# Kernel optimization log

Hardware: AMD Instinct MI355X
Metric: run time of the kernel (lower is better)

## Reference

```python
import jax, jax.numpy as jnp
from jax import lax
import numpy as np

D_MODEL = 1024
D_STATE = 16
D_CONV = 4
EXPAND = 2
D_INNER = EXPAND * D_MODEL  # 2048
DT_RANK = D_MODEL // 16     # 64
BATCH = 4
SEQ = 1024


def setup_inputs() -> dict:
    key = jax.random.key(0)
    ks = iter(jax.random.split(key, 40))
    def w(shape, s=0.02):
        return (s * jax.random.normal(next(ks), shape)).astype(jnp.float32)
    inp = {"x": jax.random.normal(next(ks), (BATCH, SEQ, D_MODEL), dtype=jnp.float32)}
    # S4D-real style A init: A = -exp(A_log), A_log = log(1..N) per channel
    Alog = jnp.log(jnp.tile(jnp.arange(1, D_STATE + 1, dtype=jnp.float32), (D_INNER, 1)))
    for s in ("f", "b"):
        inp[f"inproj_{s}"] = w((D_MODEL, 2 * D_INNER))
        inp[f"conv_w_{s}"] = w((D_INNER, D_CONV), 0.2)
        inp[f"conv_b_{s}"] = jnp.zeros((D_INNER,), jnp.float32)
        inp[f"xproj_{s}"] = w((D_INNER, DT_RANK + 2 * D_STATE))
        inp[f"dt_w_{s}"] = w((DT_RANK, D_INNER))
        inp[f"dt_b_{s}"] = jnp.full((D_INNER,), -4.0, jnp.float32)  # softplus(-4)~0.018
        inp[f"Alog_{s}"] = Alog
        inp[f"Dp_{s}"] = jnp.ones((D_INNER,), jnp.float32)
        inp[f"outproj_{s}"] = w((D_INNER, D_MODEL))
    inp["gate_w"] = w((2 * D_MODEL, D_MODEL))
    inp["gate_b"] = jnp.zeros((D_MODEL,), jnp.float32)
    inp["proj_w"] = w((D_MODEL, D_MODEL))
    inp["proj_b"] = jnp.zeros((D_MODEL,), jnp.float32)
    return inp


def _mamba(x, inproj, conv_w, conv_b, xproj, dt_w, dt_b, Alog, Dp, outproj):
    B, L, _ = x.shape
    xz = x @ inproj                           # [B,L,2*Di]
    u, z = jnp.split(xz, 2, axis=-1)          # each [B,L,Di]
    # depthwise causal conv1d, width D_CONV
    K = conv_w.shape[1]
    up = jnp.pad(u, ((0, 0), (K - 1, 0), (0, 0)))
    uc = conv_b
    for k in range(K):
        uc = uc + up[:, k:k + L, :] * conv_w[:, k]
    uc = jax.nn.silu(uc)                      # [B,L,Di]
    dbl = uc @ xproj                          # [B,L,dt_rank+2N]
    N = Alog.shape[1]
    dt, Bm, Cm = jnp.split(dbl, [DT_RANK, DT_RANK + N], axis=-1)
    delta = jax.nn.softplus(dt @ dt_w + dt_b) # [B,L,Di]
    A = -jnp.exp(Alog)                        # [Di,N]

    def step(h, inp):
        u_t, d_t, B_t, C_t = inp              # [B,Di],[B,Di],[B,N],[B,N]
        dA = jnp.exp(d_t[..., None] * A)      # [B,Di,N]
        h = dA * h + (d_t * u_t)[..., None] * B_t[:, None, :]
        y_t = jnp.einsum('bdn,bn->bd', h, C_t)
        return h, y_t

    h0 = jnp.zeros((B, uc.shape[-1], N), x.dtype)
    xs = (uc.transpose(1, 0, 2), delta.transpose(1, 0, 2),
          Bm.transpose(1, 0, 2), Cm.transpose(1, 0, 2))
    _, ys = lax.scan(step, h0, xs)            # ys: [L,B,Di]
    y = ys.transpose(1, 0, 2) + uc * Dp
    y = y * jax.nn.silu(z)
    return y @ outproj                        # [B,L,d_model]


def reference(x, inproj_f, conv_w_f, conv_b_f, xproj_f, dt_w_f, dt_b_f, Alog_f, Dp_f, outproj_f,
              inproj_b, conv_w_b, conv_b_b, xproj_b, dt_w_b, dt_b_b, Alog_b, Dp_b, outproj_b,
              gate_w, gate_b, proj_w, proj_b):
    y_f = _mamba(x, inproj_f, conv_w_f, conv_b_f, xproj_f, dt_w_f, dt_b_f, Alog_f, Dp_f, outproj_f)
    xb = jnp.flip(x, axis=1)
    y_b = _mamba(xb, inproj_b, conv_w_b, conv_b_b, xproj_b, dt_w_b, dt_b_b, Alog_b, Dp_b, outproj_b)
    y_b = jnp.flip(y_b, axis=1)
    g = jax.nn.sigmoid(jnp.concatenate([y_f, y_b], axis=-1) @ gate_w + gate_b)
    y = g * y_f + (1.0 - g) * y_b
    return y @ proj_w + proj_b
```

## Files before the change

kernel.cpp:

```cpp
#include <hip/hip_runtime.h>
#include <hip/hip_bf16.h>

#define B_  4
#define L_  1024
#define DM  1024
#define DI  2048
#define NS  16
#define RK  64
#define MT  (B_ * L_)
#define NC  32
#define CH  (L_ / NC)
#define KSX 256
#define NZX 8
#define PSZ (B_ * NC * NS * DI)

typedef unsigned short u16;
typedef __attribute__((ext_vector_type(8))) short  bh8;
typedef __attribute__((ext_vector_type(8))) unsigned short us8;
typedef __attribute__((ext_vector_type(8))) _Float16 h8;
typedef __attribute__((ext_vector_type(4))) float  f4;

__device__ __forceinline__ float bf2f(u16 u) {
  union { unsigned int i; float f; } c; c.i = ((unsigned int)u) << 16; return c.f;
}
__device__ __forceinline__ u16 f2bf(float f) {
  union { float f; unsigned int i; } c; c.f = f;
  unsigned int x = c.i;
  unsigned int r = (x + 0x7fffu + ((x >> 16) & 1u)) >> 16;
  return (u16)r;
}

__device__ __forceinline__ void gl16(const u16* g, u16* l) {
  __builtin_amdgcn_global_load_lds(
      (const __attribute__((address_space(1))) void*)g,
      (__attribute__((address_space(3))) void*)l, 16, 0, 0);
}

__global__ void detect_k(const unsigned int* __restrict__ alog,
                         int* __restrict__ flag, int* __restrict__ afl) {
  *flag = (alog[0] != 0u) ? 1 : 0;
  afl[0] = 1; afl[1] = 1;
}

__global__ __launch_bounds__(256)
void cvt_k(const void* __restrict__ src, u16* __restrict__ dst, int n,
           const int* __restrict__ flag) {
  int i = blockIdx.x * 256 + threadIdx.x;
  if (i >= n) return;
  if (*flag) dst[i] = ((const u16*)src)[i];
  else       dst[i] = f2bf(((const float*)src)[i]);
}

__global__ __launch_bounds__(256)
void cvt10_k(const int* __restrict__ flagp,
             const void* s0, u16* d0, int n0, const void* s1, u16* d1, int n1,
             const void* s2, u16* d2, int n2, const void* s3, u16* d3, int n3,
             const void* s4, u16* d4, int n4, const void* s5, u16* d5, int n5,
             const void* s6, u16* d6, int n6, const void* s7, u16* d7, int n7,
             const void* s8, u16* d8, int n8, const void* s9, u16* d9, int n9)
{
  const void* s; u16* d; int n;
  switch (blockIdx.y) {
    case 0: s = s0; d = d0; n = n0; break;  case 1: s = s1; d = d1; n = n1; break;
    case 2: s = s2; d = d2; n = n2; break;  case 3: s = s3; d = d3; n = n3; break;
    case 4: s = s4; d = d4; n = n4; break;  case 5: s = s5; d = d5; n = n5; break;
    case 6: s = s6; d = d6; n = n6; break;  case 7: s = s7; d = d7; n = n7; break;
    case 8: s = s8; d = d8; n = n8; break;  default: s = s9; d = d9; n = n9; break;
  }
  int i = blockIdx.x * 256 + threadIdx.x;
  if (i >= n) return;
  d[i] = *flagp ? ((const u16*)s)[i] : f2bf(((const float*)s)[i]);
}

__global__ __launch_bounds__(256)
void a2_k(const int* __restrict__ flagp, const void* __restrict__ sf,
          const void* __restrict__ sb, _Float16* __restrict__ A2h,
          int* __restrict__ afl)
{
  int i = blockIdx.x * 256 + threadIdx.x;
  int dir = i >> 15;
  const void* src = dir ? sb : sf;
  int j = i & (DI * NS - 1);
  float v = *flagp ? bf2f(((const u16*)src)[j]) : ((const float*)src)[j];
  float a2 = -__expf(v);
  A2h[i] = (_Float16)a2;
  int n = i & 15;
  if (fabsf(a2 + (float)(n + 1)) > 1e-3f * (n + 1)) atomicAnd(&afl[dir], 0);
}

struct TpBatch {
  const void* src[8];
  u16* dst[8];
  int R[8], C[8], tilesX[8];
  int tOff[9];
  int cnt;
};

__global__ __launch_bounds__(256)
void tposeB_k(TpBatch tb, const int* __restrict__ flag) {
  __shared__ u16 tile[32][33];
  int bid = blockIdx.x;
  int i = 0;
  #pragma unroll
  for (int q = 0; q < 7; ++q) if (i + 1 < tb.cnt && bid >= tb.tOff[i + 1]) ++i;
  int local = bid - tb.tOff[i];
  int tX = tb.tilesX[i];
  int c0 = (local % tX) * 32, r0 = (local / tX) * 32;
  int R = tb.R[i], C = tb.C[i];
  const void* src = tb.src[i];
  u16* dst = tb.dst[i];
  int tx = threadIdx.x & 31, ty = threadIdx.x >> 5;
  int isbf = *flag;
  #pragma unroll
  for (int k = 0; k < 4; ++k) {
    int r = r0 + ty + k * 8, c = c0 + tx;
    u16 v = 0;
    if (r < R && c < C)
      v = isbf ? ((const u16*)src)[(size_t)r * C + c]
               : f2bf(((const float*)src)[(size_t)r * C + c]);
    tile[ty + k * 8][tx] = v;
  }
  __syncthreads();
  #pragma unroll
  for (int k = 0; k < 4; ++k) {
    int c = c0 + ty + k * 8, r = r0 + tx;
    if (c < C && r < R)
      dst[(size_t)c * R + r] = tile[tx][ty + k * 8];
  }
}

template<int ACT, int CATM, int OUTF, int BIDIR, int SPLITK, int DUO, int XSW, int ZDIR>
__global__ __launch_bounds__(256)
void gemm2(const u16* __restrict__ A, int lda,
           const u16* __restrict__ Wt,
           const u16* __restrict__ bias,
           void* __restrict__ Cp, int ldc, void* __restrict__ C2,
           int M, int N, int K,
           const u16* __restrict__ yfp, const u16* __restrict__ ybp,
           const int* __restrict__ flagp, const u16* __restrict__ Aalt)
{
  __shared__ __align__(16) u16 As[128][64];
  __shared__ __align__(16) u16 Bs[128][64];

  int bx, by;
  if (XSW) {
    int g = blockIdx.y * gridDim.x + blockIdx.x;
    int xcd = g & 7, j = g >> 3;
    int bxb = gridDim.x >> 3;
    int sh = 31 - __builtin_clz(bxb);
    bx = xcd * bxb + (j & (bxb - 1));
    by = j >> sh;
  } else { bx = blockIdx.x; by = blockIdx.y; }

  int zdir = 0, zslice = 0;
  if (ZDIR && SPLITK) { zdir = blockIdx.z >> 3; zslice = blockIdx.z & (NZX - 1); }
  else if (ZDIR)      { zdir = blockIdx.z; }
  else if (SPLITK)    { zslice = blockIdx.z; }

  const int tid  = threadIdx.x;
  const int lane = tid & 63;
  const int w    = tid >> 6;
  const int wm   = (w >> 1) * 64, wn = (w & 1) * 64;
  const int bm0  = by * 128, bn0 = bx * 128;
  const int l15  = lane & 15, quad = lane >> 4;
  const int rI8  = lane >> 3;
  const int cG8  = (lane & 7) ^ rI8;

  const u16* Wtp = ZDIR ? (Wt + (size_t)zdir * N * K) : Wt;

  f4 acc[4][4] = {};

  const int kb = SPLITK ? zslice * KSX : 0;
  const int ke = SPLITK ? kb + KSX : K;

  for (int k0 = kb; k0 < ke; k0 += 64) {
    {
      const u16* Abase;
      if (ZDIR)     Abase = zdir ? Aalt : A;
      else if (DUO) Abase = (bn0 < DM) ? A : ybp;
      else          Abase = A;
      #pragma unroll
      for (int t = 0; t < 4; ++t) {
        int rb = w * 32 + t * 8;
        int row = rb + rI8;
        const u16* gp;
        if (CATM) {
          int kk = k0 + cG8 * 8;
          int m = bm0 + row;
          gp = (kk < DM) ? (yfp + (size_t)m * DM + kk)
                         : (ybp + (size_t)(m ^ (L_ - 1)) * DM + (kk - DM));
        } else {
          gp = Abase + (size_t)(bm0 + row) * lda + k0 + cG8 * 8;
        }
        gl16(gp, &As[rb][0]);
      }
    }
    #pragma unroll
    for (int t = 0; t < 4; ++t) {
      int rb = w * 32 + t * 8;
      int row = rb + rI8;
      int n = bn0 + row; if (n > N - 1) n = N - 1;
      gl16(Wtp + (size_t)n * K + k0 + cG8 * 8, &Bs[rb][0]);
    }
    __syncthreads();
    #pragma unroll
    for (int s = 0; s < 2; ++s) {
      bh8 af[4], bg[4];
      const int phys = ((quad + 4 * s) ^ (l15 & 7)) * 8;
      #pragma unroll
      for (int i = 0; i < 4; ++i) {
        af[i] = *(const bh8*)&As[wm + i * 16 + l15][phys];
        bg[i] = *(const bh8*)&Bs[wn + i * 16 + l15][phys];
      }
      #pragma unroll
      for (int i = 0; i < 4; ++i)
        #pragma unroll
        for (int j = 0; j < 4; ++j)
          acc[i][j] = __builtin_amdgcn_mfma_f32_16x16x32_bf16(af[i], bg[j], acc[i][j], 0, 0, 0);
    }
    __syncthreads();
  }

  const int obf = (OUTF == 1) ? *flagp : 1;
  const size_t zoff = (OUTF == 2) ? (size_t)zslice * M * ldc : 0;
  #pragma unroll
  for (int j = 0; j < 4; ++j) {
    int lcol = bn0 + wn + j * 16 + l15;
    if (lcol >= N) continue;
    int col = BIDIR ? (lcol & 4095) : (DUO ? (lcol & (DM - 1)) : lcol);
    float bv = bias ? bf2f(bias[(ZDIR ? zdir * N : 0) + col]) : 0.f;
    #pragma unroll
    for (int i = 0; i < 4; ++i) {
      #pragma unroll
      for (int r = 0; r < 4; ++r) {
        int row = bm0 + wm + i * 16 + quad * 4 + r;
        float v = acc[i][j][r] + bv;
        if (ACT == 1) v = (v > 20.f) ? v : log1pf(__expf(v));
        if (ACT == 3) {
          float g = 1.f / (1.f + __expf(-v));
          float fv = bf2f(yfp[(size_t)row * DM + col]);
          float bb = bf2f(ybp[(size_t)(row ^ (L_ - 1)) * DM + col]);
          v = g * fv + (1.f - g) * bb;
        }
        if (OUTF == 2) {
          float* base = (ZDIR && zdir) ? (float*)C2 : (float*)Cp;
          base[zoff + (size_t)row * ldc + col] = v;
        } else if (BIDIR) {
          u16* base = (lcol < 4096) ? (u16*)Cp : (u16*)C2;
          int orow = (lcol < 4096) ? row : (row ^ (L_ - 1));
          u16* dst = (col < DI) ? (base + (size_t)orow * DI + col)
                                : (base + (size_t)(8u << 20) + (size_t)orow * DI + (col - DI));
          *dst = f2bf(v);
        } else if (DUO) {
          if (lcol < DM) ((u16*)Cp)[(size_t)row * ldc + col] = f2bf(v);
          else           ((u16*)C2)[(size_t)row * ldc + col] = f2bf(v);
        } else if (ZDIR) {
          u16* base = zdir ? (u16*)C2 : (u16*)Cp;
          base[(size_t)row * ldc + col] = f2bf(v);
        } else if (OUTF == 1 && !obf) {
          ((float*)Cp)[(size_t)row * ldc + col] = v;
        } else {
          ((u16*)Cp)[(size_t)row * ldc + col] = f2bf(v);
        }
      }
    }
  }
}

__global__ __launch_bounds__(256)
void rdbl_k(const float* __restrict__ xpf, const float* __restrict__ xpb,
            u16* __restrict__ dbl)
{
  int i = blockIdx.x * 256 + threadIdx.x;
  int dir = i >= MT * 96;
  int il = dir ? (i - MT * 96) : i;
  const float* P = dir ? xpb : xpf;
  float s = 0.f;
  #pragma unroll
  for (int z = 0; z < NZX; ++z) s += P[(size_t)z * MT * 96 + il];
  dbl[i] = f2bf(s);
}

__global__ __launch_bounds__(256)
void conv8_k(const u16* __restrict__ xzu_f, const u16* __restrict__ xzu_b,
             const u16* __restrict__ cw,
             const u16* __restrict__ cb,
             u16* __restrict__ uc)
{
  int g = blockIdx.x * 256 + threadIdx.x;
  int dir = g >> 20;
  int gl = g & ((1 << 20) - 1);
  int e = gl * 8;
  int d = e & (DI - 1);
  int t = (e >> 11) & (L_ - 1);
  int b = e >> 21;
  const u16* xzu = dir ? xzu_b : xzu_f;
  const u16* cwp = cw + dir * DI * 4;
  const u16* cbp = cb + dir * DI;
  float acc[8];
  us8 cbv = *(const us8*)&cbp[d];
  #pragma unroll
  for (int i = 0; i < 8; ++i) acc[i] = bf2f(cbv[i]);
  u16 wr[32];
  #pragma unroll
  for (int q = 0; q < 4; ++q)
    *(us8*)&wr[q * 8] = *(const us8*)&cwp[d * 4 + q * 8];
  #pragma unroll
  for (int k = 0; k < 4; ++k) {
    int ts = t + k - 3;
    if (ts >= 0) {
      us8 xv = *(const us8*)&xzu[(size_t)(b * L_ + ts) * DI + d];
      #pragma unroll
      for (int i = 0; i < 8; ++i)
        acc[i] += bf2f(xv[i]) * bf2f(wr[i * 4 + k]);
    }
  }
  us8 o;
  #pragma unroll
  for (int i = 0; i < 8; ++i)
    o[i] = f2bf(acc[i] / (1.f + __expf(-acc[i])));
  *(us8*)&uc[(size_t)dir * MT * DI + e] = o;
}

__global__ __launch_bounds__(256, 4)
void scanA_k(const u16* __restrict__ delta, const u16* __restrict__ uc,
             const u16* __restrict__ dbl, const _Float16* __restrict__ A2h,
             const int* __restrict__ afl,
             _Float16* __restrict__ P, _Float16* __restrict__ S)
{
  int g = blockIdx.x * 256 + threadIdx.x;
  int dir = g >> 18;
  int gl = g & ((1 << 18) - 1);
  int d = gl & (DI - 1);
  int c = (gl >> 11) & (NC - 1);
  int b = gl >> 16;
  delta += (size_t)dir * MT * DI;
  uc    += (size_t)dir * MT * DI;
  dbl   += (size_t)dir * MT * 96;
  P     += (size_t)dir * PSZ;
  S     += (size_t)dir * PSZ;
  const int fast = afl[dir];
  float A2[NS];
  if (!fast) {
    h8 a0 = *(const h8*)&A2h[((size_t)dir * DI + d) * NS];
    h8 a1 = *(const h8*)&A2h[((size_t)dir * DI + d) * NS + 8];
    #pragma unroll
    for (int n = 0; n < 8; ++n) { A2[n] = (float)a0[n]; A2[n + 8] = (float)a1[n]; }
  }
  float Pv[NS], Sv[NS];
  #pragma unroll
  for (int n = 0; n < NS; ++n) { Pv[n] = 1.f; Sv[n] = 0.f; }
  int t0 = c * CH;
  for (int t = t0; t < t0 + CH; ++t) {
    size_t row = (size_t)b * L_ + t;
    float dv = bf2f(delta[row * DI + d]);
    float uv = bf2f(uc[row * DI + d]);
    float du = dv * uv;
    us8 b0 = *(const us8*)&dbl[row * 96 + 64];
    us8 b1 = *(const us8*)&dbl[row * 96 + 72];
    if (fast) {
      float q = __expf(-dv);
      float dA = 1.f;
      #pragma unroll
      for (int n = 0; n < NS; ++n) {
        dA *= q;
        float Bv = (n < 8) ? bf2f(b0[n & 7]) : bf2f(b1[n & 7]);
        Sv[n] = fmaf(dA, Sv[n], du * Bv);
        Pv[n] *= dA;
      }
    } else {
      #pragma unroll
      for (int n = 0; n < NS; ++n) {
        float Bv = (n < 8) ? bf2f(b0[n & 7]) : bf2f(b1[n & 7]);
        float dA = __expf(dv * A2[n]);
        Sv[n] = fmaf(dA, Sv[n], du * Bv);
        Pv[n] *= dA;
      }
    }
  }
  size_t base = ((size_t)(b * NC + c) * NS) * DI + d;
  #pragma unroll
  for (int n = 0; n < NS; ++n) {
    P[base + (size_t)n * DI] = (_Float16)Pv[n];
    S[base + (size_t)n * DI] = (_Float16)Sv[n];
  }
}

__global__ __launch_bounds__(256)
void scanB_k(_Float16* __restrict__ P, const _Float16* __restrict__ S)
{
  int g = blockIdx.x * 256 + threadIdx.x;
  int dir = g >> 17;
  int gl = g & ((1 << 17) - 1);
  int d = gl & (DI - 1);
  int n = (gl >> 11) & (NS - 1);
  int b = gl >> 15;
  P += (size_t)dir * PSZ;
  S += (size_t)dir * PSZ;
  float h = 0.f;
  #pragma unroll 4
  for (int c = 0; c < NC; ++c) {
    size_t ix = ((size_t)(b * NC + c) * NS + n) * DI + d;
    float p = (float)P[ix], s = (float)S[ix];
    P[ix] = (_Float16)h;
    h = fmaf(p, h, s);
  }
}

__global__ __launch_bounds__(256, 4)
void scanC_k(const u16* __restrict__ uc, const u16* delta,
             const u16* __restrict__ dbl, const u16* __restrict__ xzz_f,
             const u16* __restrict__ xzz_b, const _Float16* __restrict__ A2h,
             const int* __restrict__ afl, const u16* __restrict__ Dp,
             const _Float16* __restrict__ hstart, u16* ys)
{
  int g = blockIdx.x * 256 + threadIdx.x;
  int dir = g >> 18;
  int gl = g & ((1 << 18) - 1);
  int d = gl & (DI - 1);
  int c = (gl >> 11) & (NC - 1);
  int b = gl >> 16;
  const u16* xzz = dir ? xzz_b : xzz_f;
  uc     += (size_t)dir * MT * DI;
  delta  += (size_t)dir * MT * DI;
  dbl    += (size_t)dir * MT * 96;
  Dp     += dir * DI;
  hstart += (size_t)dir * PSZ;
  ys     += (size_t)dir * MT * DI;
  const int fast = afl[dir];
  float A2[NS], h[NS];
  if (!fast) {
    h8 a0 = *(const h8*)&A2h[((size_t)dir * DI + d) * NS];
    h8 a1 = *(const h8*)&A2h[((size_t)dir * DI + d) * NS + 8];
    #pragma unroll
    for (int n = 0; n < 8; ++n) { A2[n] = (float)a0[n]; A2[n + 8] = (float)a1[n]; }
  }
  float Dv = bf2f(Dp[d]);
  size_t hbase = ((size_t)(b * NC + c) * NS) * DI + d;
  #pragma unroll
  for (int n = 0; n < NS; ++n) h[n] = (float)hstart[hbase + (size_t)n * DI];
  int t0 = c * CH;
  for (int t = t0; t < t0 + CH; ++t) {
    size_t row = (size_t)b * L_ + t;
    float dv = bf2f(delta[row * DI + d]);
    float uv = bf2f(uc[row * DI + d]);
    float du = dv * uv;
    us8 b0 = *(const us8*)&dbl[row * 96 + 64];
    us8 b1 = *(const us8*)&dbl[row * 96 + 72];
    us8 c0 = *(const us8*)&dbl[row * 96 + 80];
    us8 c1 = *(const us8*)&dbl[row * 96 + 88];
    float y = 0.f;
    if (fast) {
      float q = __expf(-dv);
      float dA = 1.f;
      #pragma unroll
      for (int n = 0; n < NS; ++n) {
        dA *= q;
        float Bv = (n < 8) ? bf2f(b0[n & 7]) : bf2f(b1[n & 7]);
        float Cv = (n < 8) ? bf2f(c0[n & 7]) : bf2f(c1[n & 7]);
        h[n] = fmaf(dA, h[n], du * Bv);
        y = fmaf(h[n], Cv, y);
      }
    } else {
      #pragma unroll
      for (int n = 0; n < NS; ++n) {
        float Bv = (n < 8) ? bf2f(b0[n & 7]) : bf2f(b1[n & 7]);
        float Cv = (n < 8) ? bf2f(c0[n & 7]) : bf2f(c1[n & 7]);
        float dA = __expf(dv * A2[n]);
        h[n] = fmaf(dA, h[n], du * Bv);
        y = fmaf(h[n], Cv, y);
      }
    }
    float z = bf2f(xzz[row * DI + d]);
    float out = (y + uv * Dv) * (z / (1.f + __expf(-z)));
    ys[row * DI + d] = f2bf(out);
  }
}

extern "C" void kernel_launch(void* const* d_in, const int* in_sizes, int n_in,
                              void* d_out, int out_size, void* d_ws, size_t ws_size,
                              hipStream_t stream)
{
  char* ws = (char*)d_ws;
  const size_t MB = 1ull << 20;
  const size_t KB = 1024;

  u16* xzu_f   = (u16*)(ws + 0);
  u16* xzz_f   = (u16*)(ws + 16 * MB);
  u16* xzu_b   = (u16*)(ws + 32 * MB);
  u16* xzz_b   = (u16*)(ws + 48 * MB);
  u16* uc      = (u16*)(ws + 64 * MB);
  u16* delta_f = (u16*)(ws + 96 * MB);
  u16* delta_b = (u16*)(ws + 112 * MB);
  u16* dbl     = (u16*)(ws + 128 * MB);
  char* SM     = ws + 128 * MB + 1536 * KB;
  u16* w_convw = (u16*)(SM);
  u16* w_convb = (u16*)(SM + 32 * KB);
  u16* w_dtb   = (u16*)(SM + 40 * KB);
  u16* w_dp    = (u16*)(SM + 48 * KB);
  u16* w_gb    = (u16*)(SM + 56 * KB);
  u16* w_pb    = (u16*)(SM + 58 * KB);
  int* flag    = (int*)(SM + 60 * KB);
  int* afl     = (int*)(SM + 60 * KB + 8);
  _Float16* A2h = (_Float16*)(ws + 128 * MB + 1600 * KB);
  u16* xproj_t2 = (u16*)(ws + 128 * MB + 1728 * KB);
  u16* dtw_t2   = (u16*)(ws + 128 * MB + 2496 * KB);
  u16* xc       = uc;
  u16* inproj_t = delta_f;
  float* xpart_f = (float*)delta_f;
  float* xpart_b = (float*)delta_b;
  _Float16* Pb   = (_Float16*)xzu_f;
  _Float16* Sb   = (_Float16*)xzu_b;
  u16* outp2_t  = (u16*)(ws + 80 * MB);
  u16* gw_t     = (u16*)(ws + 88 * MB);
  u16* pw_t     = (u16*)(ws + 92 * MB);
  u16* yf       = xzz_f;
  u16* yb       = xzz_b;
  u16* yc       = (u16*)(ws + 0);

  dim3 blk(256);
  detect_k<<<1, 1, 0, stream>>>((const unsigned int*)d_in[7], flag, afl);

  cvt10_k<<<dim3(32, 10), blk, 0, stream>>>(flag,
      d_in[2],  w_convw,            DI * 4, d_in[3],  w_convb,      DI,
      d_in[6],  w_dtb,              DI,     d_in[8],  w_dp,         DI,
      d_in[11], w_convw + DI * 4,   DI * 4, d_in[12], w_convb + DI, DI,
      d_in[15], w_dtb + DI,         DI,     d_in[17], w_dp + DI,    DI,
      d_in[20], w_gb,               DM,     d_in[22], w_pb,         DM);
  a2_k<<<2 * DI * NS / 256, blk, 0, stream>>>(flag, d_in[7], d_in[16], A2h, afl);
  cvt_k<<<MT * DM / 256, blk, 0, stream>>>(d_in[0], xc, MT * DM, flag);

  {
    TpBatch tb{};
    auto add = [&](int i, const void* s, u16* d, int R, int C) {
      tb.src[i] = s; tb.dst[i] = d; tb.R[i] = R; tb.C[i] = C;
      tb.tilesX[i] = (C + 31) / 32;
      tb.tOff[i + 1] = tb.tOff[i] + tb.tilesX[i] * ((R + 31) / 32);
    };
    tb.tOff[0] = 0;
    add(0, d_in[1],  inproj_t,               DM, 2 * DI);
    add(1, d_in[10], inproj_t + 4096 * 1024, DM, 2 * DI);
    add(2, d_in[4],  xproj_t2,               DI, 96);
    add(3, d_in[13], xproj_t2 + 96 * 2048,   DI, 96);
    add(4, d_in[5],  dtw_t2,                 RK, DI);
    add(5, d_in[14], dtw_t2 + 2048 * 64,     RK, DI);
    tb.cnt = 6;
    tposeB_k<<<tb.tOff[6], blk, 0, stream>>>(tb, flag);
  }

  gemm2<0, 0, 0, 1, 0, 0, 1, 0><<<dim3(64, 32), blk, 0, stream>>>(
      xc, DM, inproj_t, nullptr, xzu_f, DI, xzu_b, MT, 2 * (2 * DI), DM,
      nullptr, nullptr, flag, nullptr);

  conv8_k<<<2 * MT * DI / 8 / 256, blk, 0, stream>>>(
      xzu_f, xzu_b, w_convw, w_convb, uc);

  gemm2<0, 0, 2, 0, 1, 0, 0, 1><<<dim3(1, 32, 2 * NZX), blk, 0, stream>>>(
      uc, DI, xproj_t2, nullptr, xpart_f, 96, xpart_b, MT, 96, DI,
      nullptr, nullptr, flag, uc + (size_t)MT * DI);
  rdbl_k<<<2 * MT * 96 / 256, blk, 0, stream>>>(xpart_f, xpart_b, dbl);

  gemm2<1, 0, 0, 0, 0, 0, 1, 1><<<dim3(16, 32, 2), blk, 0, stream>>>(
      dbl, 96, dtw_t2, w_dtb, delta_f, DI, delta_b, MT, DI, RK,
      nullptr, nullptr, flag, dbl + (size_t)MT * 96);

  scanA_k<<<2 * B_ * NC * DI / 256, blk, 0, stream>>>(
      delta_f, uc, dbl, A2h, afl, Pb, Sb);
  scanB_k<<<2 * B_ * NS * DI / 256, blk, 0, stream>>>(Pb, Sb);
  scanC_k<<<2 * B_ * NC * DI / 256, blk, 0, stream>>>(
      uc, delta_f, dbl, xzz_f, xzz_b, A2h, afl, w_dp, Pb, delta_f);

  {
    TpBatch tb{};
    auto add = [&](int i, const void* s, u16* d, int R, int C) {
      tb.src[i] = s; tb.dst[i] = d; tb.R[i] = R; tb.C[i] = C;
      tb.tilesX[i] = (C + 31) / 32;
      tb.tOff[i + 1] = tb.tOff[i] + tb.tilesX[i] * ((R + 31) / 32);
    };
    tb.tOff[0] = 0;
    add(0, d_in[9],  outp2_t,               DI, DM);
    add(1, d_in[18], outp2_t + 1024 * 2048, DI, DM);
    add(2, d_in[19], gw_t,                  2 * DM, DM);
    add(3, d_in[21], pw_t,                  DM, DM);
    tb.cnt = 4;
    tposeB_k<<<tb.tOff[4], blk, 0, stream>>>(tb, flag);
  }

  gemm2<0, 0, 0, 0, 0, 1, 1, 0><<<dim3(16, 32), blk, 0, stream>>>(
      delta_f, DI, outp2_t, nullptr, yf, DM, yb, MT, 2 * DM, DI,
      nullptr, delta_b, flag, nullptr);

  gemm2<3, 1, 0, 0, 0, 0, 1, 0><<<dim3(8, 32), blk, 0, stream>>>(
      yf, DM, gw_t, w_gb, yc, DM, nullptr, MT, DM, 2 * DM, yf, yb, flag, nullptr);
  gemm2<0, 0, 1, 0, 0, 0, 1, 0><<<dim3(8, 32), blk, 0, stream>>>(
      yc, DM, pw_t, w_pb, d_out, DM, nullptr, MT, DM, DM,
      nullptr, nullptr, flag, nullptr);
}
```

Before: 636.6 us.

## Add 256x256-tile 512-thread GEMM for bidirectional input projection

Replaces the generic gemm2 launch for the fused forward/backward input projection with a dedicated kernel. The new kernel uses 256x256 output tiles, 8 waves, a double-buffered LDS pipeline with direct global-to-LDS loads, swizzled LDS reads, and XCD-aware block remapping. The aim is more data reuse per block and better overlap of loads with MFMA work. The large tile uses 128 KB of LDS and many accumulator registers, which limits occupancy.

```diff
diff --git a/kernel.cpp b/kernel.cpp
--- a/kernel.cpp
+++ b/kernel.cpp
@@ -262,6 +262,133 @@
         } else {
           ((u16*)Cp)[(size_t)row * ldc + col] = f2bf(v);
         }
+      }
+    }
+  }
+}
+
+__global__ __launch_bounds__(512)
+void gemm256i(const u16* __restrict__ A, int lda,
+              const u16* __restrict__ Wt, int ldw,
+              u16* __restrict__ Cp, u16* __restrict__ C2, int K)
+{
+  __shared__ __align__(16) u16 As[2][256][64];
+  __shared__ __align__(16) u16 Bs[2][256][64];
+
+  int g  = blockIdx.y * gridDim.x + blockIdx.x;
+  int id = (g & 7) * ((gridDim.x * gridDim.y) >> 3) + (g >> 3);
+  int bx = id >> 4;
+  int by = id & 15;
+
+  const int tid  = threadIdx.x;
+  const int lane = tid & 63;
+  const int w    = tid >> 6;
+  const int wm2  = w >> 2;
+  const int wn4  = w & 3;
+  const int l15  = lane & 15, quad = lane >> 4;
+  const int rI8  = lane >> 3;
+  const int cG8  = (lane & 7) ^ rI8;
+  const int bm0  = by * 256, bn0 = bx * 256;
+  const int NT   = K >> 6;
+
+  const u16* Ag = A  + (size_t)(bm0 + w * 8 + rI8) * lda + cG8 * 8;
+  const u16* Bg = Wt + (size_t)(bn0 + w * 8 + rI8) * ldw + cG8 * 8;
+
+  auto STAGE = [&](int kt, int bb) {
+    const u16* ap = Ag + kt * 64;
+    const u16* bp = Bg + kt * 64;
+    #pragma unroll
+    for (int i = 0; i < 4; ++i) {
+      gl16(ap + (size_t)(i * 64) * lda, &As[bb][i * 64 + w * 8][0]);
+      gl16(bp + (size_t)(i * 64) * ldw, &Bs[bb][i * 64 + w * 8][0]);
+    }
+  };
+
+  f4 acc[8][4] = {};
+
+  STAGE(0, 0);
+  STAGE(1, 1);
+  asm volatile("s_waitcnt vmcnt(8)" ::: "memory");
+  __builtin_amdgcn_sched_barrier(0);
+  __builtin_amdgcn_s_barrier();
+
+  const int ph0 = ((quad    ) ^ (l15 & 7)) * 8;
+  const int ph1 = ((quad + 4) ^ (l15 & 7)) * 8;
+
+  for (int t = 0; t < NT; ++t) {
+    const int bb = t & 1;
+    bh8 af[4][2], bg[4][2];
+    #pragma unroll
+    for (int x = 0; x < 4; ++x) {
+      af[x][0] = *(const bh8*)&As[bb][wm2 * 128 + x * 16 + l15][ph0];
+      af[x][1] = *(const bh8*)&As[bb][wm2 * 128 + x * 16 + l15][ph1];
+      bg[x][0] = *(const bh8*)&Bs[bb][wn4 * 64  + x * 16 + l15][ph0];
+      bg[x][1] = *(const bh8*)&Bs[bb][wn4 * 64  + x * 16 + l15][ph1];
+    }
+    __builtin_amdgcn_s_setprio(1);
+    #pragma unroll
+    for (int s = 0; s < 2; ++s)
+      #pragma unroll
+      for (int i = 0; i < 4; ++i)
+        #pragma unroll
+        for (int j = 0; j < 2; ++j)
+          acc[i][j] = __builtin_amdgcn_mfma_f32_16x16x32_bf16(af[i][s], bg[j][s], acc[i][j], 0, 0, 0);
+    __builtin_amdgcn_s_setprio(0);
+    __builtin_amdgcn_s_setprio(1);
+    #pragma unroll
+    for (int s = 0; s < 2; ++s)
+      #pragma unroll
+      for (int i = 0; i < 4; ++i)
+        #pragma unroll
+        for (int j = 0; j < 2; ++j)
+          acc[i][2 + j] = __builtin_amdgcn_mfma_f32_16x16x32_bf16(af[i][s], bg[2 + j][s], acc[i][2 + j], 0, 0, 0);
+    __builtin_amdgcn_s_setprio(0);
+    #pragma unroll
+    for (int x = 0; x < 4; ++x) {
+      af[x][0] = *(const bh8*)&As[bb][wm2 * 128 + 64 + x * 16 + l15][ph0];
+      af[x][1] = *(const bh8*)&As[bb][wm2 * 128 + 64 + x * 16 + l15][ph1];
+    }
+    asm volatile("s_waitcnt lgkmcnt(0)" ::: "memory");
+    __builtin_amdgcn_sched_barrier(0);
+    __builtin_amdgcn_s_barrier();
+    if (t + 2 < NT) STAGE(t + 2, bb);
+    __builtin_amdgcn_s_setprio(1);
+    #pragma unroll
+    for (int s = 0; s < 2; ++s)
+      #pragma unroll
+      for (int i = 0; i < 4; ++i)
+        #pragma unroll
+        for (int j = 0; j < 2; ++j)
+          acc[4 + i][j] = __builtin_amdgcn_mfma_f32_16x16x32_bf16(af[i][s], bg[j][s], acc[4 + i][j], 0, 0, 0);
+    __builtin_amdgcn_s_setprio(0);
+    __builtin_amdgcn_s_setprio(1);
+    #pragma unroll
+    for (int s = 0; s < 2; ++s)
+      #pragma unroll
+      for (int i = 0; i < 4; ++i)
+        #pragma unroll
+        for (int j = 0; j < 2; ++j)
+          acc[4 + i][2 + j] = __builtin_amdgcn_mfma_f32_16x16x32_bf16(af[i][s], bg[2 + j][s], acc[4 + i][2 + j], 0, 0, 0);
+    __builtin_amdgcn_s_setprio(0);
+    if (t + 2 < NT) { asm volatile("s_waitcnt vmcnt(8)" ::: "memory"); }
+    else            { asm volatile("s_waitcnt vmcnt(0)" ::: "memory"); }
+    __builtin_amdgcn_sched_barrier(0);
+    __builtin_amdgcn_s_barrier();
+  }
+
+  #pragma unroll
+  for (int j = 0; j < 4; ++j) {
+    int lcol = bn0 + wn4 * 64 + j * 16 + l15;
+    int col  = lcol & 4095;
+    u16* base = (lcol < 4096) ? Cp : C2;
+    u16* dst0 = (col < DI) ? base : (base + (size_t)(8u << 20) - DI);
+    int flip  = (lcol < 4096) ? 0 : (L_ - 1);
+    #pragma unroll
+    for (int i = 0; i < 8; ++i) {
+      #pragma unroll
+      for (int r = 0; r < 4; ++r) {
+        int row = bm0 + wm2 * 128 + i * 16 + quad * 4 + r;
+        dst0[(size_t)(row ^ flip) * DI + col] = f2bf(acc[i][j][r]);
       }
     }
   }
@@ -548,9 +675,8 @@
     tposeB_k<<<tb.tOff[6], blk, 0, stream>>>(tb, flag);
   }
 
-  gemm2<0, 0, 0, 1, 0, 0, 1, 0><<<dim3(64, 32), blk, 0, stream>>>(
-      xc, DM, inproj_t, nullptr, xzu_f, DI, xzu_b, MT, 2 * (2 * DI), DM,
-      nullptr, nullptr, flag, nullptr);
+  gemm256i<<<dim3(32, 16), dim3(512), 0, stream>>>(
+      xc, DM, inproj_t, DM, xzu_f, xzu_b, DM);
 
   conv8_k<<<2 * MT * DI / 8 / 256, blk, 0, stream>>>(
       xzu_f, xzu_b, w_convw, w_convb, uc);
```

New measurement: 626.9 us. About the same (-1.5%).
